# Performance work log

Hardware: AMD Instinct MI355X
Metric: run time of the kernel (lower is better)

Reference implementation:

```python
import jax, jax.numpy as jnp
import numpy as np

EPS = 1e-7  # tf.keras.backend.epsilon()
R_ITER = 3

def squash(v, axis=-1):
    # Eq.(1): scale = |s|^2 / (1+|s|^2) / |s|
    s2 = jnp.sum(v * v, axis=axis, keepdims=True)
    scale = s2 / (1.0 + s2) / jnp.sqrt(s2 + EPS)
    return scale * v

def setup_inputs() -> dict:
    key = jax.random.key(0)
    k1, k2 = jax.random.split(key)
    B, Ni, Di = 64, 1152, 8
    No, Do = 64, 16
    inputs = jax.random.normal(k1, (B, Ni, Di), dtype=jnp.float32)
    # W init: tf.random.normal(stddev=0.1)
    W = 0.1 * jax.random.normal(k2, (1, Ni, No, Do, Di), dtype=jnp.float32)
    return {"inputs": inputs, "W": W}

def reference(inputs, W):
    B, Ni, Di = inputs.shape
    No, Do = W.shape[2], W.shape[3]
    # inputs_hat[b,i,o,d] = W[i,o,d,k] @ inputs[b,i,k]  (tile+matmul fused)
    u_hat = jnp.einsum('iodk,bik->biod', W[0], inputs)  # [B,Ni,No,Do]
    # raw routing logits start at shape [1,Ni,No]; broadcast to [B,...] on first update
    b_logits = jnp.zeros((1, Ni, No), dtype=inputs.dtype)
    for it in range(R_ITER):
        c = jax.nn.softmax(b_logits, axis=2)            # over output caps
        s = jnp.sum(c[..., None] * u_hat, axis=1, keepdims=True)  # [B,1,No,Do]
        v = squash(s, axis=-1)                          # [B,1,No,Do]
        if it < R_ITER - 1:
            # agreement: <u_hat, v> over capsule dim
            b_logits = b_logits + jnp.sum(u_hat * v, axis=-1)  # [B,Ni,No]
    out = jnp.squeeze(v, axis=1)                        # [B,No,Do]
    routing_weights = c[..., None, None]                # [B,Ni,No,1,1] as in TF
    return out, routing_weights
```

## Files before the change

kernel.cpp:

```cpp
#include <hip/hip_runtime.h>


#define B_      64
#define NI_     1152
#define DI_     8
#define NO_     64
#define DO_     16
#define NOD_    1024
#define CH_     96
#define CI_     12
#define BG_     8
#define BSPLIT_ 8
#define V_ELEMS 65536

static_assert(CH_ * CI_ == NI_, "chunking");
static_assert(BG_ * BSPLIT_ == B_, "b split");

template <int MODE>
__global__ __launch_bounds__(256, 3)
void caps_pass(const float* __restrict__ X,
               const float* __restrict__ W,
               const float* __restrict__ vin,
               float* __restrict__ part,
               float* __restrict__ rw)
{
    __shared__ float x_lds[BG_][CI_ * DI_];
    __shared__ float e_lds[2][BG_][NO_];
    __shared__ float invS[2][BG_];

    const int t  = threadIdx.x;
    const int o  = t >> 2, q = t & 3;
    const int ch = blockIdx.x;
    const int b0 = blockIdx.y * BG_;
    const int i0 = ch * CI_;

    const float4* wp = (const float4*)W + (size_t)i0 * 2048 + t * 8;

    float wf[4][8];
#pragma unroll
    for (int jj = 0; jj < 4; ++jj) {
        float4 a0 = wp[2 * jj], a1 = wp[2 * jj + 1];
        wf[jj][0]=a0.x; wf[jj][1]=a0.y; wf[jj][2]=a0.z; wf[jj][3]=a0.w;
        wf[jj][4]=a1.x; wf[jj][5]=a1.y; wf[jj][6]=a1.z; wf[jj][7]=a1.w;
    }
    wp += 2048;

    for (int f = t; f < BG_ * CI_ * DI_ / 4; f += 256) {
        int bb = f / (CI_ * DI_ / 4), r = f - bb * (CI_ * DI_ / 4);
        ((float4*)x_lds)[f] =
            ((const float4*)(X + ((size_t)(b0 + bb) * NI_ + i0) * DI_))[r];
    }

    float vreg[BG_][4];
    if (MODE >= 1) {
#pragma unroll
        for (int b = 0; b < BG_; ++b) {
            float4 qv = *((const float4*)(vin + (size_t)(b0 + b) * NOD_ + 4 * t));
            vreg[b][0]=qv.x; vreg[b][1]=qv.y; vreg[b][2]=qv.z; vreg[b][3]=qv.w;
        }
    }

    float acc[BG_][4];
#pragma unroll
    for (int b = 0; b < BG_; ++b) { acc[b][0]=0.f; acc[b][1]=0.f; acc[b][2]=0.f; acc[b][3]=0.f; }

    __syncthreads();

    for (int ci = 0; ci < CI_; ++ci) {
        const int i   = i0 + ci;
        const int par = ci & 1;

        float u[BG_][4];
#pragma unroll
        for (int b = 0; b < BG_; ++b) {
            const float* xb = &x_lds[b][ci * DI_];
            const float x0=xb[0],x1=xb[1],x2=xb[2],x3=xb[3];
            const float x4=xb[4],x5=xb[5],x6=xb[6],x7=xb[7];
#pragma unroll
            for (int jj = 0; jj < 4; ++jj) {
                float s = wf[jj][0] * x0;
                s = fmaf(wf[jj][1], x1, s); s = fmaf(wf[jj][2], x2, s);
                s = fmaf(wf[jj][3], x3, s); s = fmaf(wf[jj][4], x4, s);
                s = fmaf(wf[jj][5], x5, s); s = fmaf(wf[jj][6], x6, s);
                s = fmaf(wf[jj][7], x7, s);
                u[b][jj] = s;
            }
            if (MODE >= 1) {
                float a = u[b][0]*vreg[b][0] + u[b][1]*vreg[b][1]
                        + u[b][2]*vreg[b][2] + u[b][3]*vreg[b][3];
                a += __shfl_xor(a, 1);
                a += __shfl_xor(a, 2);
                if (q == 0) e_lds[par][b][o] = __expf(a);
            } else {
                acc[b][0]+=u[b][0]; acc[b][1]+=u[b][1];
                acc[b][2]+=u[b][2]; acc[b][3]+=u[b][3];
            }
        }

        if (ci + 1 < CI_) {
#pragma unroll
            for (int jj = 0; jj < 4; ++jj) {
                float4 a0 = wp[2 * jj], a1 = wp[2 * jj + 1];
                wf[jj][0]=a0.x; wf[jj][1]=a0.y; wf[jj][2]=a0.z; wf[jj][3]=a0.w;
                wf[jj][4]=a1.x; wf[jj][5]=a1.y; wf[jj][6]=a1.z; wf[jj][7]=a1.w;
            }
            wp += 2048;
        }

        if (MODE >= 1) {
            __syncthreads();
            {
                const int bb = t >> 5, l = t & 31;
                float s = e_lds[par][bb][l] + e_lds[par][bb][l + 32];
                s += __shfl_xor(s, 1);  s += __shfl_xor(s, 2);  s += __shfl_xor(s, 4);
                s += __shfl_xor(s, 8);  s += __shfl_xor(s, 16);
                if (l == 0) invS[par][bb] = 1.0f / s;
            }
            __syncthreads();
#pragma unroll
            for (int b = 0; b < BG_; ++b) {
                const float c = e_lds[par][b][o] * invS[par][b];
                acc[b][0] = fmaf(c, u[b][0], acc[b][0]);
                acc[b][1] = fmaf(c, u[b][1], acc[b][1]);
                acc[b][2] = fmaf(c, u[b][2], acc[b][2]);
                acc[b][3] = fmaf(c, u[b][3], acc[b][3]);
                if (MODE == 2 && q == 0)
                    rw[((size_t)(b0 + b) * NI_ + i) * NO_ + o] = c;
            }
        }
    }

#pragma unroll
    for (int b = 0; b < BG_; ++b) {
        float4 val;
        val.x=acc[b][0]; val.y=acc[b][1]; val.z=acc[b][2]; val.w=acc[b][3];
        *((float4*)(part + (((size_t)(b0 + b) * CH_ + ch) * NOD_ + 4 * t))) = val;
    }
}

template <int MODE>
__global__ __launch_bounds__(128)
void caps_squash(const float* __restrict__ part, const float* __restrict__ v0in,
                 float* __restrict__ vout)
{
    const int c4 = blockIdx.x * 128 + threadIdx.x;
    const int b = c4 >> 8, od4 = c4 & 255;
    const float4* p = (const float4*)part + (size_t)b * CH_ * 256 + od4;
    float4 s = {0.f, 0.f, 0.f, 0.f};
#pragma unroll 8
    for (int ch = 0; ch < CH_; ++ch) {
        float4 q = p[(size_t)ch * 256];
        s.x += q.x; s.y += q.y; s.z += q.z; s.w += q.w;
    }
    if (MODE == 0) { s.x*=(1.f/64.f); s.y*=(1.f/64.f); s.z*=(1.f/64.f); s.w*=(1.f/64.f); }
    float s2 = s.x*s.x + s.y*s.y + s.z*s.z + s.w*s.w;
    s2 += __shfl_xor(s2, 1); s2 += __shfl_xor(s2, 2);
    const float scale = s2 / ((1.0f + s2) * sqrtf(s2 + 1e-7f));
    float4 v; v.x = scale*s.x; v.y = scale*s.y; v.z = scale*s.z; v.w = scale*s.w;
    if (MODE == 1) {
        float4 v0 = ((const float4*)v0in)[c4];
        v.x += v0.x; v.y += v0.y; v.z += v0.z; v.w += v0.w;
    }
    ((float4*)vout)[c4] = v;
}

__global__ __launch_bounds__(1024, 1)
void caps_naive(const float* __restrict__ X, const float* __restrict__ W,
                float* __restrict__ outv, float* __restrict__ outc)
{
    __shared__ float xs[NI_ * DI_];
    __shared__ float agree[NO_];
    __shared__ float expo[NO_];
    __shared__ float s2sh[NO_];
    __shared__ float den;

    const int b = blockIdx.x, tid = threadIdx.x;
    const int o = tid >> 4, d = tid & 15;

    for (int f = tid; f < NI_ * DI_; f += 1024)
        xs[f] = X[(size_t)b * NI_ * DI_ + f];
    __syncthreads();

    float vprev = 0.f, v0 = 0.f, vout = 0.f;
    for (int phase = 0; phase < 3; ++phase) {
        float sacc = 0.f;
        for (int i = 0; i < NI_; ++i) {
            const float* wp = W + (size_t)i * 8192 + (size_t)tid * 8;
            const float* xp = xs + i * DI_;
            float u = 0.f;
#pragma unroll
            for (int k = 0; k < 8; ++k) u = fmaf(wp[k], xp[k], u);
            if (phase == 0) { sacc += u; continue; }
            if (d == 0) agree[o] = 0.f;
            __syncthreads();
            atomicAdd(&agree[o], u * vprev);
            __syncthreads();
            if (tid == 0) den = 0.f;
            __syncthreads();
            if (d == 0) { float e = __expf(agree[o]); expo[o] = e; atomicAdd(&den, e); }
            __syncthreads();
            float c = expo[o] / den;
            sacc = fmaf(c, u, sacc);
            if (phase == 2 && d == 0)
                outc[((size_t)b * NI_ + i) * NO_ + o] = c;
            __syncthreads();
        }
        if (phase == 0) sacc *= (1.0f / 64.0f);
        if (d == 0) s2sh[o] = 0.f;
        __syncthreads();
        atomicAdd(&s2sh[o], sacc * sacc);
        __syncthreads();
        const float s2 = s2sh[o];
        const float scale = s2 / ((1.0f + s2) * sqrtf(s2 + 1e-7f));
        const float vv = scale * sacc;
        if (phase == 0)      { v0 = vv; vprev = vv; }
        else if (phase == 1) { vprev = v0 + vv; }
        else                 { vout = vv; }
        __syncthreads();
    }
    outv[(size_t)b * (NO_ * DO_) + tid] = vout;
}

extern "C" void kernel_launch(void* const* d_in, const int* in_sizes, int n_in,
                              void* d_out, int out_size, void* d_ws, size_t ws_size,
                              hipStream_t stream)
{
    const float *X, *W;
    if (in_sizes[0] < in_sizes[1]) { X = (const float*)d_in[0]; W = (const float*)d_in[1]; }
    else                           { X = (const float*)d_in[1]; W = (const float*)d_in[0]; }

    float* out  = (float*)d_out;
    float* outv = out;
    float* outc = out + V_ELEMS;

    const size_t needBig = ((size_t)B_ * CH_ * NOD_ + 2 * (size_t)B_ * NOD_) * sizeof(float);
    if (ws_size < needBig) {
        caps_naive<<<B_, 1024, 0, stream>>>(X, W, outv, outc);
        return;
    }

    float* part = (float*)d_ws;
    float* v0   = part + (size_t)B_ * CH_ * NOD_;
    float* w01  = v0 + (size_t)B_ * NOD_;

    dim3 gP(CH_, BSPLIT_), blk(256), gS(128), blkS(128);
    caps_pass<0><<<gP, blk, 0, stream>>>(X, W, nullptr, part, nullptr);
    caps_squash<0><<<gS, blkS, 0, stream>>>(part, nullptr, v0);
    caps_pass<1><<<gP, blk, 0, stream>>>(X, W, v0, part, nullptr);
    caps_squash<1><<<gS, blkS, 0, stream>>>(part, v0, w01);
    caps_pass<2><<<gP, blk, 0, stream>>>(X, W, w01, part, outc);
    caps_squash<2><<<gS, blkS, 0, stream>>>(part, nullptr, outv);
}
```

Measured before the change: 255.9 us.

## Share W tiles across batch groups via LDS in 1024-thread blocks

Each block now has 1024 threads in four 8-batch groups. They cooperatively stage each capsule's W slice into a padded LDS tile, with the next slice's global loads prefetched into registers. Each block covers 32 batches instead of 8, so W is read from global memory twice per pass instead of eight times. Chunking changes from 96×12 to 128×9, and __syncthreads is replaced by a raw s_barrier with an lgkmcnt wait. The cost is an extra barrier on every capsule step, one large block per CU with lower occupancy, a bigger workspace for partial sums, and more partials for the squash kernel to sum.

```diff
diff --git a/kernel.cpp b/kernel.cpp
--- a/kernel.cpp
+++ b/kernel.cpp
@@ -7,73 +7,101 @@
 #define NO_     64
 #define DO_     16
 #define NOD_    1024
-#define CH_     96
-#define CI_     12
-#define BG_     8
-#define BSPLIT_ 8
+#define CH_     128
+#define CI_     9
+#define BGT_    8
+#define NG_     4
+#define BGB_    32
+#define BSPLIT_ 2
 #define V_ELEMS 65536
+#define PADR    33
 
 static_assert(CH_ * CI_ == NI_, "chunking");
-static_assert(BG_ * BSPLIT_ == B_, "b split");
+static_assert(BGB_ * BSPLIT_ == B_, "b split");
+
+#define RAW_BARRIER() do { \
+    asm volatile("s_waitcnt lgkmcnt(0)" ::: "memory"); \
+    __builtin_amdgcn_s_barrier(); \
+    __builtin_amdgcn_sched_barrier(0); } while (0)
 
 template <int MODE>
-__global__ __launch_bounds__(256, 3)
+__global__ __launch_bounds__(1024, 4)
 void caps_pass(const float* __restrict__ X,
                const float* __restrict__ W,
                const float* __restrict__ vin,
                float* __restrict__ part,
                float* __restrict__ rw)
 {
-    __shared__ float x_lds[BG_][CI_ * DI_];
-    __shared__ float e_lds[2][BG_][NO_];
-    __shared__ float invS[2][BG_];
+    __shared__ float4 wtile[NO_ * PADR];
+    __shared__ float  x_lds[BGB_][CI_ * DI_];
+    __shared__ float  e_lds[2][BGB_][NO_];
+    __shared__ float  invS[2][BGB_];
 
     const int t  = threadIdx.x;
-    const int o  = t >> 2, q = t & 3;
+    const int o  = (t >> 2) & 63, q = t & 3, g = t >> 8;
     const int ch = blockIdx.x;
-    const int b0 = blockIdx.y * BG_;
+    const int bg0 = blockIdx.y * BGB_;
     const int i0 = ch * CI_;
 
-    const float4* wp = (const float4*)W + (size_t)i0 * 2048 + t * 8;
-
-    float wf[4][8];
-#pragma unroll
-    for (int jj = 0; jj < 4; ++jj) {
-        float4 a0 = wp[2 * jj], a1 = wp[2 * jj + 1];
-        wf[jj][0]=a0.x; wf[jj][1]=a0.y; wf[jj][2]=a0.z; wf[jj][3]=a0.w;
-        wf[jj][4]=a1.x; wf[jj][5]=a1.y; wf[jj][6]=a1.z; wf[jj][7]=a1.w;
-    }
-    wp += 2048;
-
-    for (int f = t; f < BG_ * CI_ * DI_ / 4; f += 256) {
-        int bb = f / (CI_ * DI_ / 4), r = f - bb * (CI_ * DI_ / 4);
-        ((float4*)x_lds)[f] =
-            ((const float4*)(X + ((size_t)(b0 + bb) * NI_ + i0) * DI_))[r];
-    }
-
-    float vreg[BG_][4];
+    const float4* Wq = (const float4*)W;
+
+    float4 tmp0, tmp1;
+    {
+        const float4* wg = Wq + (size_t)i0 * 2048;
+        tmp0 = wg[t]; tmp1 = wg[t + 1024];
+    }
+
+    if (t < BGB_ * CI_ * DI_ / 4) {
+        const int bb = t / (CI_ * DI_ / 4), r = t - bb * (CI_ * DI_ / 4);
+        ((float4*)x_lds)[t] =
+            ((const float4*)(X + ((size_t)(bg0 + bb) * NI_ + i0) * DI_))[r];
+    }
+
+    float vreg[BGT_][4];
     if (MODE >= 1) {
 #pragma unroll
-        for (int b = 0; b < BG_; ++b) {
-            float4 qv = *((const float4*)(vin + (size_t)(b0 + b) * NOD_ + 4 * t));
+        for (int b = 0; b < BGT_; ++b) {
+            float4 qv = *((const float4*)(vin + (size_t)(bg0 + g * BGT_ + b) * NOD_
+                                          + 4 * (t & 255)));
             vreg[b][0]=qv.x; vreg[b][1]=qv.y; vreg[b][2]=qv.z; vreg[b][3]=qv.w;
         }
     }
 
-    float acc[BG_][4];
-#pragma unroll
-    for (int b = 0; b < BG_; ++b) { acc[b][0]=0.f; acc[b][1]=0.f; acc[b][2]=0.f; acc[b][3]=0.f; }
-
-    __syncthreads();
+    float acc[BGT_][4];
+#pragma unroll
+    for (int b = 0; b < BGT_; ++b) { acc[b][0]=0.f; acc[b][1]=0.f; acc[b][2]=0.f; acc[b][3]=0.f; }
+
+    RAW_BARRIER();
 
     for (int ci = 0; ci < CI_; ++ci) {
         const int i   = i0 + ci;
         const int par = ci & 1;
 
-        float u[BG_][4];
-#pragma unroll
-        for (int b = 0; b < BG_; ++b) {
-            const float* xb = &x_lds[b][ci * DI_];
+        wtile[(t >> 5) * PADR + (t & 31)] = tmp0;
+        {
+            const int f = t + 1024;
+            wtile[(f >> 5) * PADR + (f & 31)] = tmp1;
+        }
+        RAW_BARRIER();
+
+        if (ci + 1 < CI_) {
+            const float4* wg = Wq + (size_t)(i + 1) * 2048;
+            tmp0 = wg[t]; tmp1 = wg[t + 1024];
+        }
+
+        float wf[4][8];
+#pragma unroll
+        for (int jj = 0; jj < 4; ++jj) {
+            float4 a0 = wtile[o * PADR + 8 * q + 2 * jj];
+            float4 a1 = wtile[o * PADR + 8 * q + 2 * jj + 1];
+            wf[jj][0]=a0.x; wf[jj][1]=a0.y; wf[jj][2]=a0.z; wf[jj][3]=a0.w;
+            wf[jj][4]=a1.x; wf[jj][5]=a1.y; wf[jj][6]=a1.z; wf[jj][7]=a1.w;
+        }
+
+        float u[BGT_][4];
+#pragma unroll
+        for (int b = 0; b < BGT_; ++b) {
+            const float* xb = &x_lds[g * BGT_ + b][ci * DI_];
             const float x0=xb[0],x1=xb[1],x2=xb[2],x3=xb[3];
             const float x4=xb[4],x5=xb[5],x6=xb[6],x7=xb[7];
 #pragma unroll
@@ -90,25 +118,15 @@
                         + u[b][2]*vreg[b][2] + u[b][3]*vreg[b][3];
                 a += __shfl_xor(a, 1);
                 a += __shfl_xor(a, 2);
-                if (q == 0) e_lds[par][b][o] = __expf(a);
+                if (q == 0) e_lds[par][g * BGT_ + b][o] = __expf(a);
             } else {
                 acc[b][0]+=u[b][0]; acc[b][1]+=u[b][1];
                 acc[b][2]+=u[b][2]; acc[b][3]+=u[b][3];
             }
         }
 
-        if (ci + 1 < CI_) {
-#pragma unroll
-            for (int jj = 0; jj < 4; ++jj) {
-                float4 a0 = wp[2 * jj], a1 = wp[2 * jj + 1];
-                wf[jj][0]=a0.x; wf[jj][1]=a0.y; wf[jj][2]=a0.z; wf[jj][3]=a0.w;
-                wf[jj][4]=a1.x; wf[jj][5]=a1.y; wf[jj][6]=a1.z; wf[jj][7]=a1.w;
-            }
-            wp += 2048;
-        }
-
         if (MODE >= 1) {
-            __syncthreads();
+            RAW_BARRIER();
             {
                 const int bb = t >> 5, l = t & 31;
                 float s = e_lds[par][bb][l] + e_lds[par][bb][l + 32];
@@ -116,25 +134,28 @@
                 s += __shfl_xor(s, 8);  s += __shfl_xor(s, 16);
                 if (l == 0) invS[par][bb] = 1.0f / s;
             }
-            __syncthreads();
-#pragma unroll
-            for (int b = 0; b < BG_; ++b) {
-                const float c = e_lds[par][b][o] * invS[par][b];
+            RAW_BARRIER();
+#pragma unroll
+            for (int b = 0; b < BGT_; ++b) {
+                const float c = e_lds[par][g * BGT_ + b][o] * invS[par][g * BGT_ + b];
                 acc[b][0] = fmaf(c, u[b][0], acc[b][0]);
                 acc[b][1] = fmaf(c, u[b][1], acc[b][1]);
                 acc[b][2] = fmaf(c, u[b][2], acc[b][2]);
                 acc[b][3] = fmaf(c, u[b][3], acc[b][3]);
                 if (MODE == 2 && q == 0)
-                    rw[((size_t)(b0 + b) * NI_ + i) * NO_ + o] = c;
-            }
-        }
-    }
-
-#pragma unroll
-    for (int b = 0; b < BG_; ++b) {
+                    rw[((size_t)(bg0 + g * BGT_ + b) * NI_ + i) * NO_ + o] = c;
+            }
+        } else {
+            RAW_BARRIER();
+        }
+    }
+
+#pragma unroll
+    for (int b = 0; b < BGT_; ++b) {
         float4 val;
         val.x=acc[b][0]; val.y=acc[b][1]; val.z=acc[b][2]; val.w=acc[b][3];
-        *((float4*)(part + (((size_t)(b0 + b) * CH_ + ch) * NOD_ + 4 * t))) = val;
+        *((float4*)(part + (((size_t)(bg0 + g * BGT_ + b) * CH_ + ch) * NOD_
+                            + 4 * (t & 255)))) = val;
     }
 }
 
@@ -243,7 +264,7 @@
     float* v0   = part + (size_t)B_ * CH_ * NOD_;
     float* w01  = v0 + (size_t)B_ * NOD_;
 
-    dim3 gP(CH_, BSPLIT_), blk(256), gS(128), blkS(128);
+    dim3 gP(CH_, BSPLIT_), blk(1024), gS(128), blkS(128);
     caps_pass<0><<<gP, blk, 0, stream>>>(X, W, nullptr, part, nullptr);
     caps_squash<0><<<gS, blkS, 0, stream>>>(part, nullptr, v0);
     caps_pass<1><<<gP, blk, 0, stream>>>(X, W, v0, part, nullptr);
```

After: 356.6 us. 1.39x slower.
